# Performance work log

Measured on AMD Instinct MI355X. Metric: run time of the kernel, lower is better.

Reference implementation:

```python
import math
import jax, jax.numpy as jnp
import numpy as np

N = 100_000          # nodes
D = 128              # sample.num_node_features
E = 1_600_000        # edges (avg degree 16)
ACM = 4              # augmented_channels_multiplier
C = 128              # channels = 4*4*channels_optuna(=8)
RATIO = 0.7          # topk_ratio + 0.1
FINAL_NODES = 3


def setup_inputs() -> dict:
    key = jax.random.key(0)
    ks = jax.random.split(key, 14)
    s = 0.05
    x = jax.random.normal(ks[0], (N, D), jnp.float32)
    edge_index = jax.random.randint(ks[1], (2, E), 0, N, dtype=jnp.int32)
    # dense_input GraphConv(D, ACM): called with empty edges -> only lin_root weight + lin_rel bias matter
    Wd_root = jax.random.normal(ks[2], (ACM, D), jnp.float32) * s
    bd = jax.random.normal(ks[3], (ACM,), jnp.float32) * s
    # input GraphConv(ACM, C)
    Wi_rel = jax.random.normal(ks[4], (C, ACM), jnp.float32) * s
    bi = jax.random.normal(ks[5], (C,), jnp.float32) * s
    Wi_root = jax.random.normal(ks[6], (C, ACM), jnp.float32) * s
    # TopKPooling(C) attention vector
    p = jax.random.normal(ks[7], (C,), jnp.float32) * s
    # conv1 GraphConv(C, 2C)
    W1_rel = jax.random.normal(ks[8], (2 * C, C), jnp.float32) * s
    b1 = jax.random.normal(ks[9], (2 * C,), jnp.float32) * s
    W1_root = jax.random.normal(ks[10], (2 * C, C), jnp.float32) * s
    # output Linear(3 * 2C, 1)
    Wo = jax.random.normal(ks[11], (1, FINAL_NODES * 2 * C), jnp.float32) * s
    bo = jax.random.normal(ks[12], (1,), jnp.float32) * s
    return {"x": x, "edge_index": edge_index, "Wd_root": Wd_root, "bd": bd,
            "Wi_rel": Wi_rel, "bi": bi, "Wi_root": Wi_root, "p": p,
            "W1_rel": W1_rel, "b1": b1, "W1_root": W1_root, "Wo": Wo, "bo": bo}


def reference(x, edge_index, Wd_root, bd, Wi_rel, bi, Wi_root, p, W1_rel, b1, W1_root, Wo, bo):
    n = x.shape[0]
    src, dst = edge_index[0], edge_index[1]  # messages flow src -> dst

    # dense_input GraphConv with empty edge set: aggr == 0 -> lin_rel bias + lin_root(x)
    h = jax.nn.gelu(x @ Wd_root.T + bd, approximate=False)               # [N, ACM]

    # input GraphConv(ACM, C): out = lin_rel(sum_j x_j) + lin_root(x)
    aggr = jax.ops.segment_sum(h[src], dst, num_segments=n)              # [N, ACM]
    h = jax.nn.gelu(aggr @ Wi_rel.T + bi + h @ Wi_root.T, approximate=False)  # [N, C]

    # TopKPooling(C, ratio=0.7): score = tanh(x.p / ||p||), keep top-k, scale kept x by score
    k = int(math.ceil(RATIO * n))
    score = jnp.tanh((h @ p) / jnp.linalg.norm(p))                        # [N]
    top_scores, perm = jax.lax.top_k(score, k)
    hp = h[perm] * top_scores[:, None]                                    # [k, C]
    # remap edges: kept node -> new index, dropped -> sentinel k
    inv = jnp.full((n,), k, dtype=jnp.int32).at[perm].set(jnp.arange(k, dtype=jnp.int32))
    ns, nd = inv[src], inv[dst]
    valid = (ns < k) & (nd < k)

    # conv1 GraphConv(C, 2C) on coarsened graph (masked scatter, sentinel row dropped)
    msg = jnp.where(valid[:, None], hp[jnp.minimum(ns, k - 1)], 0.0)      # [E, C]
    aggr = jax.ops.segment_sum(msg, jnp.where(valid, nd, k), num_segments=k + 1)[:k]
    h2 = jax.nn.gelu(aggr @ W1_rel.T + b1 + hp @ W1_root.T, approximate=False)  # [k, 2C]

    # avg_pool_x with cluster = i % 3 over single-graph batch
    cluster = jnp.arange(k, dtype=jnp.int32) % FINAL_NODES
    sums = jax.ops.segment_sum(h2, cluster, num_segments=FINAL_NODES)
    counts = jax.ops.segment_sum(jnp.ones((k,), h2.dtype), cluster, num_segments=FINAL_NODES)
    pooled = sums / counts[:, None]                                       # [3, 2C]

    # output Linear on flattened vector -> shape [1]
    return pooled.reshape(-1) @ Wo.T + bo
```

## Files before the change

### kernel.cpp

```cpp
#include <hip/hip_runtime.h>
#include <stdint.h>

#define N_NODES 100000
#define D_FEAT  128
#define E_EDGES 1600000
#define ACMC    4
#define CCH     128
#define C2CH    256
#define KKEEP   70000
#define KPAD    70016
#define NBLK    (KPAD / 64)
#define BINCAP  64
#define NBINS   (1 << 20)
#define NWIN    8
#define WWIN    12500

typedef unsigned int u32;
typedef unsigned long long u64;
typedef unsigned short u16;
typedef short bf16x8 __attribute__((ext_vector_type(8)));
typedef float f32x4 __attribute__((ext_vector_type(4)));
typedef int i32x4 __attribute__((ext_vector_type(4)));

__device__ __forceinline__ float gelu_exact(float v){
    return 0.5f * v * (1.0f + erff(v * 0.70710678118654752440f));
}
__device__ __forceinline__ float bflo(u32 v){ return __uint_as_float(v << 16); }
__device__ __forceinline__ float bfhi(u32 v){ return __uint_as_float(v & 0xFFFF0000u); }
__device__ __forceinline__ u16 f2bf(float f){
    u32 x = __float_as_uint(f);
    return (u16)((x + 0x7FFFu + ((x >> 16) & 1u)) >> 16);
}

__global__ __launch_bounds__(256) void k_build(const int* __restrict__ ei,
                                               int* __restrict__ deg,
                                               int* __restrict__ slot) {
    int b = blockIdx.x;
    int win = b & (NWIN - 1);
    int chunk = b >> 3;
    int e0 = (chunk * 256 + threadIdx.x) * 4;
    if (e0 >= E_EDGES) return;
    i32x4 dv = __builtin_nontemporal_load((const i32x4*)(ei + E_EDGES + e0));
    i32x4 sv = __builtin_nontemporal_load((const i32x4*)(ei + e0));
    int lo = win * WWIN, hi = lo + WWIN;
    #pragma unroll
    for (int j = 0; j < 4; j++) {
        int d = dv[j];
        if (d >= lo && d < hi) {
            int pos = atomicAdd(&deg[d], 1);
            if (pos < BINCAP) slot[d * BINCAP + pos] = sv[j];
        }
    }
}

__global__ __launch_bounds__(256) void k_h1(const float* __restrict__ x,
                                            const float* __restrict__ Wd,
                                            const float* __restrict__ bd,
                                            float* __restrict__ h1) {
    int tid = threadIdx.x;
    int wid = tid >> 6, lane = tid & 63;
    int node = blockIdx.x * 4 + wid;
    if (node >= N_NODES) return;
    const float2* xr = (const float2*)(x + (size_t)node * D_FEAT);
    float2 v = xr[lane];
    const float2* wd = (const float2*)Wd;
    float s[4];
    #pragma unroll
    for (int j = 0; j < 4; j++) {
        float2 w = wd[j * 64 + lane];
        s[j] = v.x * w.x + v.y * w.y;
    }
    #pragma unroll
    for (int off = 32; off > 0; off >>= 1) {
        #pragma unroll
        for (int j = 0; j < 4; j++) s[j] += __shfl_xor(s[j], off);
    }
    if (lane == 0) {
        float4 o;
        o.x = gelu_exact(s[0] + bd[0]);
        o.y = gelu_exact(s[1] + bd[1]);
        o.z = gelu_exact(s[2] + bd[2]);
        o.w = gelu_exact(s[3] + bd[3]);
        ((float4*)h1)[node] = o;
    }
}

__global__ __launch_bounds__(256) void k_aggr1g(const int* __restrict__ deg,
                                                const int* __restrict__ slot,
                                                const float* __restrict__ h1,
                                                float* __restrict__ aggr1) {
    int d = blockIdx.x * blockDim.x + threadIdx.x;
    if (d >= N_NODES) return;
    int cnt = deg[d]; if (cnt > BINCAP) cnt = BINCAP;
    int base = d * BINCAP;
    float4 acc = make_float4(0.f, 0.f, 0.f, 0.f);
    for (int i0 = 0; i0 < cnt; i0 += 8) {
        int m = cnt - i0; if (m > 8) m = 8;
        int ss[8];
        #pragma unroll
        for (int j = 0; j < 8; j++) {
            int sj = slot[base + i0 + j];
            ss[j] = (j < m) ? sj : 0;
        }
        float4 vv[8];
        #pragma unroll
        for (int j = 0; j < 8; j++) vv[j] = ((const float4*)h1)[ss[j]];
        #pragma unroll
        for (int j = 0; j < 8; j++) {
            float msk = (j < m) ? 1.f : 0.f;
            acc.x += msk * vv[j].x;
            acc.y += msk * vv[j].y;
            acc.z += msk * vv[j].z;
            acc.w += msk * vv[j].w;
        }
    }
    ((float4*)aggr1)[d] = acc;
}

__global__ __launch_bounds__(128) void k_h_score(const float* __restrict__ aggr1,
                                                 const float* __restrict__ h1,
                                                 const float* __restrict__ Wi_rel,
                                                 const float* __restrict__ bi,
                                                 const float* __restrict__ Wi_root,
                                                 const float* __restrict__ p,
                                                 u16* __restrict__ hsb,
                                                 u32* __restrict__ dkey,
                                                 int* __restrict__ hist) {
    int node = blockIdx.x;
    int c = threadIdx.x;
    float4 ag = ((const float4*)aggr1)[node];
    float4 hv = ((const float4*)h1)[node];
    float4 wr = ((const float4*)Wi_rel)[c];
    float4 wo = ((const float4*)Wi_root)[c];
    float val = ag.x * wr.x + ag.y * wr.y + ag.z * wr.z + ag.w * wr.w
              + hv.x * wo.x + hv.y * wo.y + hv.z * wo.z + hv.w * wo.w
              + bi[c];
    float g = gelu_exact(val);
    float pc = p[c];
    float hp = g * pc, pp = pc * pc;
    #pragma unroll
    for (int off = 32; off > 0; off >>= 1) {
        hp += __shfl_xor(hp, off);
        pp += __shfl_xor(pp, off);
    }
    __shared__ float sh[2], sp[2];
    __shared__ float sscore;
    int wid = c >> 6, lane = c & 63;
    if (lane == 0) { sh[wid] = hp; sp[wid] = pp; }
    __syncthreads();
    if (c == 0) {
        float H = sh[0] + sh[1], P = sp[0] + sp[1];
        float sc = tanhf(H / sqrtf(P));
        sscore = sc;
        u32 u = __float_as_uint(sc);
        u32 asc = (u & 0x80000000u) ? ~u : (u | 0x80000000u);
        u32 d = ~asc;
        dkey[node] = d;
        atomicAdd(&hist[d >> 12], 1);
    }
    __syncthreads();
    hsb[(size_t)node * CCH + c] = f2bf(g * sscore);
}

__global__ __launch_bounds__(1024) void k_scan1(const int* __restrict__ hist,
                                                int* __restrict__ cursor,
                                                int* __restrict__ bsum) {
    __shared__ int s[1024];
    int t = threadIdx.x;
    int g = blockIdx.x * 1024 + t;
    int v = hist[g];
    s[t] = v;
    __syncthreads();
    #pragma unroll
    for (int off = 1; off < 1024; off <<= 1) {
        int o = (t >= off) ? s[t - off] : 0;
        __syncthreads();
        s[t] += o;
        __syncthreads();
    }
    cursor[g] = s[t] - v;
    if (t == 1023) bsum[blockIdx.x] = s[t];
}

__global__ __launch_bounds__(1024) void k_scan2(int* __restrict__ bsum) {
    __shared__ int s[1024];
    int t = threadIdx.x;
    int v = bsum[t];
    s[t] = v;
    __syncthreads();
    #pragma unroll
    for (int off = 1; off < 1024; off <<= 1) {
        int o = (t >= off) ? s[t - off] : 0;
        __syncthreads();
        s[t] += o;
        __syncthreads();
    }
    bsum[t] = s[t] - v;
}

__global__ __launch_bounds__(1024) void k_scan3(int* __restrict__ cursor,
                                                const int* __restrict__ bsum) {
    int t = threadIdx.x;
    int g = blockIdx.x * 1024 + t;
    cursor[g] += bsum[blockIdx.x];
}

__global__ __launch_bounds__(256) void k_scatter(const u32* __restrict__ dkey,
                                                 int* __restrict__ cursor,
                                                 u64* __restrict__ out64) {
    int i = blockIdx.x * blockDim.x + threadIdx.x;
    if (i >= N_NODES) return;
    u32 d = dkey[i];
    int pos = atomicAdd(&cursor[d >> 12], 1);
    out64[pos] = (((u64)d) << 32) | (u32)i;
}

__global__ __launch_bounds__(256) void k_refine(const u64* __restrict__ out64,
                                                const int* __restrict__ cursor,
                                                const int* __restrict__ hist,
                                                int* __restrict__ rank,
                                                int* __restrict__ noder) {
    int pp = blockIdx.x * blockDim.x + threadIdx.x;
    if (pp >= N_NODES) return;
    u64 kp = out64[pp];
    u32 b = (u32)(kp >> 44);
    int end = cursor[b];
    int cnt = hist[b];
    int start = end - cnt;
    int r = start;
    if (cnt > 1) {
        int c = 0;
        for (int q = start; q < end; q++) c += (out64[q] < kp) ? 1 : 0;
        r = start + c;
    }
    int node = (int)(u32)kp;
    rank[node] = r;
    noder[r] = node;
}

__global__ __launch_bounds__(256) void k_gather(const int* __restrict__ deg,
                                                const int* __restrict__ slot,
                                                const int* __restrict__ rank,
                                                const u32* __restrict__ hsb32,
                                                u32* __restrict__ inb32) {
    int tid = threadIdx.x;
    int wid = tid >> 6, lane = tid & 63;
    int d = blockIdx.x * 4 + wid;
    if (d >= N_NODES) return;
    int rd = rank[d];
    if (rd >= KKEEP) return;
    int cnt = deg[d]; if (cnt > BINCAP) cnt = BINCAP;
    int base = d * BINCAP;
    float ax = 0.f, ay = 0.f;
    for (int i0 = 0; i0 < cnt; i0 += 16) {
        int m = cnt - i0; if (m > 16) m = 16;
        int ss[16];
        #pragma unroll
        for (int j = 0; j < 16; j++) {
            int sj = slot[base + i0 + j];
            ss[j] = (j < m) ? sj : 0;
        }
        int rr[16];
        u32 vv[16];
        #pragma unroll
        for (int j = 0; j < 16; j++) {
            rr[j] = rank[ss[j]];
            vv[j] = hsb32[(size_t)ss[j] * 64 + lane];
        }
        #pragma unroll
        for (int j = 0; j < 16; j++) {
            float msk = (j < m && rr[j] < KKEEP) ? 1.f : 0.f;
            ax += msk * bflo(vv[j]);
            ay += msk * bfhi(vv[j]);
        }
    }
    inb32[(size_t)rd * 128 + lane] = (u32)f2bf(ax) | ((u32)f2bf(ay) << 16);
}

__global__ __launch_bounds__(256) void k_pack(const int* __restrict__ noder,
                                              const u32* __restrict__ hsb32,
                                              u32* __restrict__ inb32) {
    int tid = threadIdx.x;
    int wave = tid >> 6, lane = tid & 63;
    int r = blockIdx.x * 4 + wave;
    if (r >= KPAD) return;
    if (r < KKEEP) {
        int n = noder[r];
        inb32[(size_t)r * 128 + 64 + lane] = hsb32[(size_t)n * 64 + lane];
    } else {
        inb32[(size_t)r * 128 + lane] = 0;
        inb32[(size_t)r * 128 + 64 + lane] = 0;
    }
}

__global__ __launch_bounds__(128) void k_wconv(const float* __restrict__ Wrel,
                                               const float* __restrict__ Wroot,
                                               u16* __restrict__ wcat) {
    int ch = blockIdx.x, t = threadIdx.x;
    wcat[(size_t)ch * 256 + t]       = f2bf(Wrel[(size_t)ch * 128 + t]);
    wcat[(size_t)ch * 256 + 128 + t] = f2bf(Wroot[(size_t)ch * 128 + t]);
}

__global__ __launch_bounds__(256) void k_h2mfma(const u16* __restrict__ inb,
                                                const u16* __restrict__ wcat,
                                                const float* __restrict__ b1,
                                                float* __restrict__ partial) {
    __shared__ float ps[768];
    int tid = threadIdx.x;
    int lane = tid & 63, wave = tid >> 6;
    int blk = blockIdx.x;
    for (int i = tid; i < 768; i += 256) ps[i] = 0.f;
    __syncthreads();

    int col = lane & 15, quad = lane >> 4;
    int rbase = blk * 64 + wave * 16;
    const bf16x8* arow = (const bf16x8*)(inb + (size_t)(rbase + col) * 256 + quad * 8);
    bf16x8 a[8];
    #pragma unroll
    for (int k0 = 0; k0 < 8; k0++) a[k0] = arow[k0 * 4];

    #pragma unroll 1
    for (int ct = 0; ct < 16; ct++) {
        int ch = ct * 16 + col;
        const bf16x8* brow = (const bf16x8*)(wcat + (size_t)ch * 256 + quad * 8);
        f32x4 acc = {0.f, 0.f, 0.f, 0.f};
        #pragma unroll
        for (int k0 = 0; k0 < 8; k0++)
            acc = __builtin_amdgcn_mfma_f32_16x16x32_bf16(a[k0], brow[k0 * 4], acc, 0, 0, 0);
        float b = b1[ch];
        float p0 = 0.f, p1 = 0.f, p2 = 0.f;
        #pragma unroll
        for (int reg = 0; reg < 4; reg++) {
            int r = rbase + quad * 4 + reg;
            float g = (r < KKEEP) ? gelu_exact(acc[reg] + b) : 0.f;
            int m = r % 3;
            if (m == 0) p0 += g; else if (m == 1) p1 += g; else p2 += g;
        }
        p0 += __shfl_xor(p0, 16); p0 += __shfl_xor(p0, 32);
        p1 += __shfl_xor(p1, 16); p1 += __shfl_xor(p1, 32);
        p2 += __shfl_xor(p2, 16); p2 += __shfl_xor(p2, 32);
        if (quad == 0) {
            atomicAdd(&ps[0 * 256 + ch], p0);
            atomicAdd(&ps[1 * 256 + ch], p1);
            atomicAdd(&ps[2 * 256 + ch], p2);
        }
    }
    __syncthreads();
    for (int i = tid; i < 768; i += 256)
        partial[(size_t)blk * 768 + i] = ps[i];
}

__global__ __launch_bounds__(64) void k_poolred(const float* __restrict__ partial,
                                                float* __restrict__ pooled) {
    int j = blockIdx.x;
    int lane = threadIdx.x;
    float s = 0.f;
    for (int i = lane; i < NBLK; i += 64)
        s += partial[(size_t)i * 768 + j];
    #pragma unroll
    for (int off = 32; off > 0; off >>= 1) s += __shfl_xor(s, off);
    if (lane == 0) pooled[j] = s;
}

__global__ __launch_bounds__(768) void k_out(const float* __restrict__ pooled,
                                             const float* __restrict__ Wo,
                                             const float* __restrict__ bo,
                                             float* __restrict__ out) {
    __shared__ float red[12];
    int t = threadIdx.x;
    int ci = t >> 8;
    float cnt = (ci == 0) ? 23334.0f : 23333.0f;
    float acc = (pooled[t] / cnt) * Wo[t];
    #pragma unroll
    for (int off = 32; off > 0; off >>= 1) acc += __shfl_xor(acc, off);
    int wid = t >> 6, lane = t & 63;
    if (lane == 0) red[wid] = acc;
    __syncthreads();
    if (t == 0) {
        float s = 0.0f;
        #pragma unroll
        for (int w = 0; w < 12; w++) s += red[w];
        out[0] = s + bo[0];
    }
}

extern "C" void kernel_launch(void* const* d_in, const int* in_sizes, int n_in,
                              void* d_out, int out_size, void* d_ws, size_t ws_size,
                              hipStream_t stream) {
    const float* x       = (const float*)d_in[0];
    const int*   ei      = (const int*)d_in[1];
    const float* Wd      = (const float*)d_in[2];
    const float* bd      = (const float*)d_in[3];
    const float* Wi_rel  = (const float*)d_in[4];
    const float* bi      = (const float*)d_in[5];
    const float* Wi_root = (const float*)d_in[6];
    const float* p       = (const float*)d_in[7];
    const float* W1_rel  = (const float*)d_in[8];
    const float* b1      = (const float*)d_in[9];
    const float* W1_root = (const float*)d_in[10];
    const float* Wo      = (const float*)d_in[11];
    const float* bo      = (const float*)d_in[12];

    char* ws = (char*)d_ws;
    size_t off_b = 0;
    auto alloc = [&](size_t bytes) -> void* {
        void* ptr = ws + off_b;
        off_b += (bytes + 255) & ~(size_t)255;
        return ptr;
    };
    float* h1     = (float*)alloc((size_t)N_NODES * 4 * sizeof(float));
    float* aggr1  = (float*)alloc((size_t)N_NODES * 4 * sizeof(float));
    u16*   hsb    = (u16*)alloc((size_t)N_NODES * CCH * sizeof(u16));
    u32*   dkey   = (u32*)alloc((size_t)N_NODES * sizeof(u32));
    int*   rank   = (int*)alloc((size_t)N_NODES * sizeof(int));
    int*   noder  = (int*)alloc((size_t)N_NODES * sizeof(int));
    int*   deg    = (int*)alloc((size_t)N_NODES * sizeof(int));
    int*   slot   = (int*)alloc((size_t)N_NODES * BINCAP * sizeof(int));
    u16*   inb    = (u16*)alloc((size_t)KPAD * C2CH * sizeof(u16));
    u16*   wcat   = (u16*)alloc((size_t)C2CH * 256 * sizeof(u16));
    float* partial= (float*)alloc((size_t)NBLK * 768 * sizeof(float));
    float* pooled = (float*)alloc(768 * sizeof(float));
    (void)ws_size; (void)in_sizes; (void)n_in; (void)out_size;

    int* hist   = (int*)inb;
    int* cursor = (int*)inb + NBINS;
    u64* out64  = (u64*)((int*)inb + 2 * NBINS);
    int* bsum   = (int*)(out64 + N_NODES);

    hipMemsetAsync(deg, 0, (size_t)N_NODES * sizeof(int), stream);
    hipMemsetAsync(hist, 0, (size_t)NBINS * sizeof(int), stream);

    k_build<<<1563 * NWIN, 256, 0, stream>>>(ei, deg, slot);
    k_wconv<<<256, 128, 0, stream>>>(W1_rel, W1_root, wcat);

    k_h1<<<N_NODES / 4, 256, 0, stream>>>(x, Wd, bd, h1);
    k_aggr1g<<<(N_NODES + 255) / 256, 256, 0, stream>>>(deg, slot, h1, aggr1);
    k_h_score<<<N_NODES, 128, 0, stream>>>(aggr1, h1, Wi_rel, bi, Wi_root, p,
                                           hsb, dkey, hist);

    k_scan1<<<NBINS / 1024, 1024, 0, stream>>>(hist, cursor, bsum);
    k_scan2<<<1, 1024, 0, stream>>>(bsum);
    k_scan3<<<NBINS / 1024, 1024, 0, stream>>>(cursor, bsum);
    k_scatter<<<(N_NODES + 255) / 256, 256, 0, stream>>>(dkey, cursor, out64);
    k_refine<<<(N_NODES + 255) / 256, 256, 0, stream>>>(out64, cursor, hist, rank, noder);

    k_gather<<<(N_NODES + 3) / 4, 256, 0, stream>>>(deg, slot, rank,
                                                    (const u32*)hsb, (u32*)inb);
    k_pack<<<(KPAD + 3) / 4, 256, 0, stream>>>(noder, (const u32*)hsb, (u32*)inb);
    k_h2mfma<<<NBLK, 256, 0, stream>>>(inb, wcat, b1, partial);
    k_poolred<<<768, 64, 0, stream>>>(partial, pooled);
    k_out<<<1, 768, 0, stream>>>(pooled, Wo, bo, (float*)d_out);
}
```

Before: 450.4 us.

## Stage swizzled weight matrix in LDS and enlarge MFMA register tile per wave

The conv1 MFMA kernel now copies the full concatenated bf16 weight matrix (256x256) into LDS once per block, using an XOR swizzle to avoid bank conflicts. Blocks grow to 512 threads covering 128 rows, and each wave computes a 32x128 tile with 16 accumulators instead of 16x16 tiles looped over channel tiles. The aim is to cut repeated global/L2 weight reads and raise MFMA reuse of the A and B fragments. In exchange it uses about 131KB of LDS per block, which limits occupancy to one block per CU, and raises register pressure.

Result: faster. 437.2 us (-2.9%).

```diff
diff --git a/kernel.cpp b/kernel.cpp
--- a/kernel.cpp
+++ b/kernel.cpp
@@ -9,7 +9,7 @@
 #define C2CH    256
 #define KKEEP   70000
 #define KPAD    70016
-#define NBLK    (KPAD / 64)
+#define NBLK    547
 #define BINCAP  64
 #define NBINS   (1 << 20)
 #define NWIN    8
@@ -301,52 +301,95 @@
     wcat[(size_t)ch * 256 + 128 + t] = f2bf(Wroot[(size_t)ch * 128 + t]);
 }
 
-__global__ __launch_bounds__(256) void k_h2mfma(const u16* __restrict__ inb,
-                                                const u16* __restrict__ wcat,
-                                                const float* __restrict__ b1,
-                                                float* __restrict__ partial) {
+__global__ __launch_bounds__(512, 2) void k_h2mfma(const u16* __restrict__ inb,
+                                                   const u16* __restrict__ wcat,
+                                                   const float* __restrict__ b1,
+                                                   float* __restrict__ partial) {
+    __shared__ u16 bs[256 * 256];
     __shared__ float ps[768];
     int tid = threadIdx.x;
+    int blk = blockIdx.x;
+
+    {
+        int ch = tid >> 1;
+        int seg = tid & 1;
+        const char* src = (const char*)wcat + (size_t)ch * 512 + seg * 256;
+        char* dst = (char*)bs + (size_t)ch * 512;
+        int swz = (ch & 7) << 4;
+        #pragma unroll
+        for (int i = 0; i < 16; i++) {
+            int k = seg * 256 + i * 16;
+            *(i32x4*)(dst + (k ^ swz)) = *(const i32x4*)(src + i * 16);
+        }
+    }
+    for (int i = tid; i < 768; i += 512) ps[i] = 0.f;
+    __syncthreads();
+
     int lane = tid & 63, wave = tid >> 6;
-    int blk = blockIdx.x;
-    for (int i = tid; i < 768; i += 256) ps[i] = 0.f;
-    __syncthreads();
-
+    int wm = wave >> 1, wn = wave & 1;
     int col = lane & 15, quad = lane >> 4;
-    int rbase = blk * 64 + wave * 16;
-    const bf16x8* arow = (const bf16x8*)(inb + (size_t)(rbase + col) * 256 + quad * 8);
-    bf16x8 a[8];
-    #pragma unroll
-    for (int k0 = 0; k0 < 8; k0++) a[k0] = arow[k0 * 4];
-
-    #pragma unroll 1
-    for (int ct = 0; ct < 16; ct++) {
-        int ch = ct * 16 + col;
-        const bf16x8* brow = (const bf16x8*)(wcat + (size_t)ch * 256 + quad * 8);
-        f32x4 acc = {0.f, 0.f, 0.f, 0.f};
+    int rbase = blk * 128 + wm * 32;
+    int chbase = wn * 128;
+
+    bf16x8 a[2][8];
+    #pragma unroll
+    for (int m = 0; m < 2; m++) {
+        const char* ar = (const char*)inb + (size_t)(rbase + m * 16 + col) * 512 + quad * 16;
         #pragma unroll
         for (int k0 = 0; k0 < 8; k0++)
-            acc = __builtin_amdgcn_mfma_f32_16x16x32_bf16(a[k0], brow[k0 * 4], acc, 0, 0, 0);
-        float b = b1[ch];
-        float p0 = 0.f, p1 = 0.f, p2 = 0.f;
-        #pragma unroll
-        for (int reg = 0; reg < 4; reg++) {
-            int r = rbase + quad * 4 + reg;
-            float g = (r < KKEEP) ? gelu_exact(acc[reg] + b) : 0.f;
-            int m = r % 3;
-            if (m == 0) p0 += g; else if (m == 1) p1 += g; else p2 += g;
-        }
-        p0 += __shfl_xor(p0, 16); p0 += __shfl_xor(p0, 32);
-        p1 += __shfl_xor(p1, 16); p1 += __shfl_xor(p1, 32);
-        p2 += __shfl_xor(p2, 16); p2 += __shfl_xor(p2, 32);
-        if (quad == 0) {
-            atomicAdd(&ps[0 * 256 + ch], p0);
-            atomicAdd(&ps[1 * 256 + ch], p1);
-            atomicAdd(&ps[2 * 256 + ch], p2);
-        }
-    }
-    __syncthreads();
-    for (int i = tid; i < 768; i += 256)
+            a[m][k0] = *(const bf16x8*)(ar + k0 * 64);
+    }
+
+    f32x4 acc[2][8];
+    #pragma unroll
+    for (int m = 0; m < 2; m++)
+        #pragma unroll
+        for (int n = 0; n < 8; n++)
+            acc[m][n] = (f32x4){0.f, 0.f, 0.f, 0.f};
+
+    int swzr = (col & 7) << 4;
+    #pragma unroll
+    for (int k0 = 0; k0 < 8; k0++) {
+        int kb = k0 * 64 + quad * 16;
+        bf16x8 b[8];
+        #pragma unroll
+        for (int n = 0; n < 8; n++) {
+            int ch = chbase + n * 16 + col;
+            b[n] = *(const bf16x8*)((const char*)bs + (size_t)ch * 512 + (kb ^ swzr));
+        }
+        #pragma unroll
+        for (int n = 0; n < 8; n++) {
+            acc[0][n] = __builtin_amdgcn_mfma_f32_16x16x32_bf16(a[0][k0], b[n], acc[0][n], 0, 0, 0);
+            acc[1][n] = __builtin_amdgcn_mfma_f32_16x16x32_bf16(a[1][k0], b[n], acc[1][n], 0, 0, 0);
+        }
+    }
+
+    #pragma unroll
+    for (int m = 0; m < 2; m++) {
+        #pragma unroll
+        for (int n = 0; n < 8; n++) {
+            int ch = chbase + n * 16 + col;
+            float bias = b1[ch];
+            float p0 = 0.f, p1 = 0.f, p2 = 0.f;
+            #pragma unroll
+            for (int reg = 0; reg < 4; reg++) {
+                int r = rbase + m * 16 + quad * 4 + reg;
+                float g = (r < KKEEP) ? gelu_exact(acc[m][n][reg] + bias) : 0.f;
+                int md = r % 3;
+                if (md == 0) p0 += g; else if (md == 1) p1 += g; else p2 += g;
+            }
+            p0 += __shfl_xor(p0, 16); p0 += __shfl_xor(p0, 32);
+            p1 += __shfl_xor(p1, 16); p1 += __shfl_xor(p1, 32);
+            p2 += __shfl_xor(p2, 16); p2 += __shfl_xor(p2, 32);
+            if (quad == 0) {
+                atomicAdd(&ps[0 * 256 + ch], p0);
+                atomicAdd(&ps[1 * 256 + ch], p1);
+                atomicAdd(&ps[2 * 256 + ch], p2);
+            }
+        }
+    }
+    __syncthreads();
+    for (int i = tid; i < 768; i += 512)
         partial[(size_t)blk * 768 + i] = ps[i];
 }
 
@@ -447,7 +490,7 @@
     k_gather<<<(N_NODES + 3) / 4, 256, 0, stream>>>(deg, slot, rank,
                                                     (const u32*)hsb, (u32*)inb);
     k_pack<<<(KPAD + 3) / 4, 256, 0, stream>>>(noder, (const u32*)hsb, (u32*)inb);
-    k_h2mfma<<<NBLK, 256, 0, stream>>>(inb, wcat, b1, partial);
+    k_h2mfma<<<NBLK, 512, 0, stream>>>(inb, wcat, b1, partial);
     k_poolred<<<768, 64, 0, stream>>>(partial, pooled);
     k_out<<<1, 768, 0, stream>>>(pooled, Wo, bo, (float*)d_out);
 }
```
